# Performance work log

Hardware: AMD Instinct MI355X
Metric: run time of the kernel (lower is better)

## Reference

```python
import jax, jax.numpy as jnp
import numpy as np

N_HEADS, D_MODEL, D_HEAD, N_CTX = 16, 2048, 128, 2048
BATCH, SEQ = 2, 2048
ATTN_SCALE = float(np.sqrt(D_HEAD))
IGNORE = -100000.0


def setup_inputs() -> dict:
    key = jax.random.key(0)
    ks = jax.random.split(key, 6)
    init = 0.02
    return {
        "residual": jax.random.normal(ks[0], (BATCH, SEQ, D_MODEL), dtype=jnp.float32),
        "x": jax.random.normal(ks[1], (BATCH, SEQ, D_MODEL), dtype=jnp.float32),
        "W_Q": jax.random.normal(ks[2], (N_HEADS, D_MODEL, D_HEAD), dtype=jnp.float32) * init,
        "W_K": jax.random.normal(ks[3], (N_HEADS, D_MODEL, D_HEAD), dtype=jnp.float32) * init,
        "W_V": jax.random.normal(ks[4], (N_HEADS, D_MODEL, D_HEAD), dtype=jnp.float32) * init,
        "W_O": jax.random.normal(ks[5], (N_HEADS, D_HEAD, D_MODEL), dtype=jnp.float32) * init,
        "b_Q": jnp.zeros((N_HEADS, D_HEAD), dtype=jnp.float32),
        "b_K": jnp.zeros((N_HEADS, D_HEAD), dtype=jnp.float32),
        "b_V": jnp.zeros((N_HEADS, D_HEAD), dtype=jnp.float32),
        "b_O": jnp.zeros((D_MODEL,), dtype=jnp.float32),
    }


def reference(residual, x, W_Q, W_K, W_V, W_O, b_Q, b_K, b_V, b_O):
    # use_split_qkv_input=False: QKV all read from residual
    q = jnp.einsum('bpm,hmd->bphd', residual, W_Q) + b_Q  # [b, pos, h, d_head]
    k = jnp.einsum('bpm,hmd->bphd', residual, W_K) + b_K
    v = jnp.einsum('bpm,hmd->bphd', residual, W_V) + b_V
    attn_scores = jnp.einsum('bqhd,bkhd->bhqk', q, k) / ATTN_SCALE  # [b, h, q, k]
    key_len = attn_scores.shape[-1]
    mask = jnp.tril(jnp.ones((key_len, key_len), dtype=bool))  # causal mask [q, k]
    attn_scores = jnp.where(mask, attn_scores, IGNORE)
    pattern = jax.nn.softmax(attn_scores, axis=-1)
    z = jnp.einsum('bkhd,bhqk->bqhd', v, pattern)
    out = jnp.einsum('bphd,hdm->bpm', z, W_O) + b_O
    return (residual, out)
```

## Files before the change

### kernel.cpp

```cpp
#include <hip/hip_runtime.h>
#include <hip/hip_bf16.h>

typedef __attribute__((ext_vector_type(8))) short bf16x8;
typedef __attribute__((ext_vector_type(4))) float f32x4;

#define N_HEADS 16
#define D_MODEL 2048
#define D_HEAD  128
#define SEQ     2048
#define BATCH   2
#define HD      (N_HEADS * D_HEAD)
#define QSCALE  0.08838834764831845f

__device__ inline __hip_bfloat16 to_bf16(float v) { return __float2bfloat16(v); }
__device__ inline __hip_bfloat16 to_bf16(__hip_bfloat16 v) { return v; }

typedef __attribute__((address_space(3))) unsigned lds_u32_t;
typedef __attribute__((address_space(1))) unsigned glb_u32_t;
__device__ inline void async16(void* l, const void* g) {
    __builtin_amdgcn_global_load_lds((const glb_u32_t*)g, (lds_u32_t*)l, 16, 0, 0);
}

__global__ __launch_bounds__(256) void cvt_dual(
    const float4* __restrict__ in, float4* __restrict__ o32,
    __hip_bfloat16* __restrict__ obf, long n4)
{
    for (long i = (long)blockIdx.x * blockDim.x + threadIdx.x; i < n4;
         i += (long)gridDim.x * blockDim.x) {
        float4 v = in[i];
        o32[i] = v;
        union { __hip_bfloat16 b[4]; uint2 u; } p;
        p.b[0] = __float2bfloat16(v.x);
        p.b[1] = __float2bfloat16(v.y);
        p.b[2] = __float2bfloat16(v.z);
        p.b[3] = __float2bfloat16(v.w);
        *(uint2*)(obf + 4 * i) = p.u;
    }
}

template <typename Tin>
__global__ __launch_bounds__(256) void transpose_to_bf16(
    const Tin* __restrict__ in, __hip_bfloat16* __restrict__ out,
    int R, int C, long in_rs, long in_bs, long out_bs)
{
    __shared__ Tin tile[64][65];
    const Tin* src = in + (long)blockIdx.z * in_bs;
    __hip_bfloat16* dst = out + (long)blockIdx.z * out_bs;
    const int c0 = blockIdx.x * 64, r0 = blockIdx.y * 64;
    const int t = threadIdx.x;
    const int tr = t >> 4;
    const int tc = (t & 15) * 4;
#pragma unroll
    for (int i = 0; i < 4; i++) {
        int r = tr + i * 16;
#pragma unroll
        for (int j = 0; j < 4; j++)
            tile[r][tc + j] = src[(long)(r0 + r) * in_rs + c0 + tc + j];
    }
    __syncthreads();
#pragma unroll
    for (int i = 0; i < 4; i++) {
        int c = tr + i * 16;
#pragma unroll
        for (int j = 0; j < 4; j++)
            dst[(long)(c0 + c) * R + r0 + tc + j] = to_bf16(tile[tc + j][c]);
    }
}

__device__ inline void store_out(__hip_bfloat16* p, float v) { *p = __float2bfloat16(v); }
__device__ inline void store_out(float* p, float v) { *p = v; }

template <typename OutT>
__global__ __launch_bounds__(256) void gemm_qkv(
    const __hip_bfloat16* __restrict__ A,
    const __hip_bfloat16* __restrict__ WTbase,
    const float* __restrict__ bQ, const float* bK, const float* bV,
    OutT* __restrict__ Cbase,
    int M, int N, int K, long wstride, long cstride, float scale0)
{
    __shared__ __align__(16) __hip_bfloat16 As[128 * 32];
    __shared__ __align__(16) __hip_bfloat16 Bs[128 * 32];
    const int z = blockIdx.z;
    const __hip_bfloat16* Bt = WTbase + (long)z * wstride;
    const float* bias = (z == 0) ? bQ : ((z == 1) ? bK : bV);
    OutT* C = Cbase + (long)z * cstride;
    const float outscale = (z == 0) ? scale0 : 1.0f;

    const int tid = threadIdx.x;
    const int lane = tid & 63, wave = tid >> 6;
    const int l15 = lane & 15, quad = lane >> 4;
    const int wr = wave >> 1, wc = wave & 1;
    const int m0 = blockIdx.y * 128, n0 = blockIdx.x * 128;

    const short* Ap = (const short*)A;
    const short* Bp = (const short*)Bt;

    f32x4 acc[4][4] = {};

    for (int k0 = 0; k0 < K; k0 += 32) {
        __syncthreads();
#pragma unroll
        for (int i = 0; i < 2; i++) {
            int e = i * 256 + tid;
            int row = e >> 2, ch = e & 3;
            async16((char*)As + (i * 256 + wave * 64) * 16,
                    Ap + (long)(m0 + row) * K + k0 + ch * 8);
            async16((char*)Bs + (i * 256 + wave * 64) * 16,
                    Bp + (long)(n0 + row) * K + k0 + ch * 8);
        }
        __syncthreads();

        bf16x8 af[4], bfr[4];
#pragma unroll
        for (int t = 0; t < 4; t++) {
            af[t]  = *(const bf16x8*)((const short*)As + (wr * 64 + t * 16 + l15) * 32 + quad * 8);
            bfr[t] = *(const bf16x8*)((const short*)Bs + (wc * 64 + t * 16 + l15) * 32 + quad * 8);
        }
#pragma unroll
        for (int i = 0; i < 4; i++)
#pragma unroll
            for (int j = 0; j < 4; j++)
                acc[i][j] = __builtin_amdgcn_mfma_f32_16x16x32_bf16(af[i], bfr[j], acc[i][j], 0, 0, 0);
    }

    const int mw = m0 + wr * 64, nw = n0 + wc * 64;
#pragma unroll
    for (int i = 0; i < 4; i++) {
#pragma unroll
        for (int j = 0; j < 4; j++) {
            int n = nw + j * 16 + l15;
            float bv = bias[n];
#pragma unroll
            for (int r = 0; r < 4; r++) {
                int m = mw + i * 16 + quad * 4 + r;
                store_out(&C[(long)m * N + n], (acc[i][j][r] + bv) * outscale);
            }
        }
    }
}

template <typename OutT>
__global__ __launch_bounds__(256, 2) void gemm128(
    const __hip_bfloat16* __restrict__ A,
    const __hip_bfloat16* __restrict__ WTbase,
    const float* __restrict__ bQ, const float* bK, const float* bV,
    OutT* __restrict__ Cbase,
    int N, int K, long wstride, long cstride, float scale0,
    int nx, int ny)
{
    __shared__ __align__(16) short lds[2][2][128 * 64];

    const int tid = threadIdx.x;
    const int lane = tid & 63;
    const int wave = tid >> 6;
    const int l15 = lane & 15, quad = lane >> 4, l7 = lane & 7;
    const int wm = wave >> 1, wn = wave & 1;

    const int nwg = gridDim.x;
    const int orig = blockIdx.x;
    const int wg = (orig & 7) * (nwg >> 3) + (orig >> 3);
    const int nxy = nx * ny;
    const int z = wg / nxy;
    const int rem = wg - z * nxy;
    const int by = rem / nx;
    const int bx = rem - by * nx;
    const int m0 = by * 128, n0 = bx * 128;

    const short* Ap = (const short*)A;
    const short* Bp = (const short*)WTbase + (long)z * wstride;

    const int rsub = lane >> 3;
    const int c0 = (lane & 7) ^ rsub;

    auto stage = [&](int bf, int reg, const short* gbase, int kt) {
        char* base = (char*)&lds[bf][reg][0];
        const short* g = gbase + (long)kt * 64;
#pragma unroll
        for (int s = 0; s < 4; s++) {
            int row = (s * 4 + wave) * 8 + rsub;
            async16(base + (s * 4 + wave) * 1024, g + (long)row * K + c0 * 8);
        }
    };

    const short* Agbl = Ap + (long)m0 * K;
    const short* Bgbl = Bp + (long)n0 * K;

    const int NT = K >> 6;

    stage(0, 0, Agbl, 0); stage(0, 1, Bgbl, 0);
    stage(1, 0, Agbl, 1);
    asm volatile("s_waitcnt vmcnt(4)" ::: "memory");
    __builtin_amdgcn_s_barrier();

    f32x4 acc[4][4] = {};
    const int ar0 = wm * 64;
    const int br0 = wn * 64;

#pragma unroll 2
    for (int u = 0; u < NT; ++u) {
        asm volatile("" ::: "memory");
        const int bf = u & 1, bo = bf ^ 1;
        const short* la = &lds[bf][0][0];
        const short* lb = &lds[bf][1][0];

        bf16x8 a[4][2], b0[2][2], b1[2][2];

#pragma unroll
        for (int fm = 0; fm < 4; fm++)
#pragma unroll
            for (int kk = 0; kk < 2; kk++)
                a[fm][kk] = *(const bf16x8*)(la + (ar0 + fm * 16 + l15) * 64
                                             + (((kk * 4 + quad) ^ l7) * 8));
#pragma unroll
        for (int fn = 0; fn < 2; fn++)
#pragma unroll
            for (int kk = 0; kk < 2; kk++)
                b0[fn][kk] = *(const bf16x8*)(lb + (br0 + fn * 16 + l15) * 64
                                              + (((kk * 4 + quad) ^ l7) * 8));
        if (u + 1 < NT) stage(bo, 1, Bgbl, u + 1);
        __builtin_amdgcn_s_barrier();
        asm volatile("s_waitcnt lgkmcnt(0)" ::: "memory");
        __builtin_amdgcn_sched_barrier(0);
        __builtin_amdgcn_s_setprio(1);
#pragma unroll
        for (int fm = 0; fm < 4; fm++)
#pragma unroll
            for (int fn = 0; fn < 2; fn++)
#pragma unroll
                for (int kk = 0; kk < 2; kk++)
                    acc[fm][fn] = __builtin_amdgcn_mfma_f32_16x16x32_bf16(
                        a[fm][kk], b0[fn][kk], acc[fm][fn], 0, 0, 0);
        __builtin_amdgcn_s_setprio(0);
        __builtin_amdgcn_s_barrier();

#pragma unroll
        for (int fn = 0; fn < 2; fn++)
#pragma unroll
            for (int kk = 0; kk < 2; kk++)
                b1[fn][kk] = *(const bf16x8*)(lb + (br0 + 32 + fn * 16 + l15) * 64
                                              + (((kk * 4 + quad) ^ l7) * 8));
        if (u + 2 < NT) stage(bf, 0, Agbl, u + 2);
        __builtin_amdgcn_s_barrier();
        asm volatile("s_waitcnt lgkmcnt(0)" ::: "memory");
        __builtin_amdgcn_sched_barrier(0);
        __builtin_amdgcn_s_setprio(1);
#pragma unroll
        for (int fm = 0; fm < 4; fm++)
#pragma unroll
            for (int fn = 0; fn < 2; fn++)
#pragma unroll
                for (int kk = 0; kk < 2; kk++)
                    acc[fm][2 + fn] = __builtin_amdgcn_mfma_f32_16x16x32_bf16(
                        a[fm][kk], b1[fn][kk], acc[fm][2 + fn], 0, 0, 0);
        __builtin_amdgcn_s_setprio(0);
        if (u + 2 < NT) {
            asm volatile("s_waitcnt vmcnt(4)" ::: "memory");
        } else if (u + 1 < NT) {
            asm volatile("s_waitcnt vmcnt(0)" ::: "memory");
        }
        __builtin_amdgcn_s_barrier();
    }

    const float* bias = (z == 0) ? bQ : ((z == 1) ? bK : bV);
    OutT* C = Cbase + (long)z * cstride;
    const float outscale = (z == 0) ? scale0 : 1.0f;
#pragma unroll
    for (int mi = 0; mi < 4; mi++) {
#pragma unroll
        for (int nj = 0; nj < 4; nj++) {
            const int n = n0 + wn * 64 + nj * 16 + l15;
            const float bv = bias[n];
#pragma unroll
            for (int r = 0; r < 4; r++) {
                const int m = m0 + wm * 64 + mi * 16 + quad * 4 + r;
                store_out(&C[(long)m * N + n], (acc[mi][nj][r] + bv) * outscale);
            }
        }
    }
}

__global__ __launch_bounds__(512, 4) void attn_fused(
    const __hip_bfloat16* Q,
    const __hip_bfloat16* __restrict__ Kin,
    const __hip_bfloat16* __restrict__ Vt,
    __hip_bfloat16* Z)
{
    __shared__ __align__(16) __hip_bfloat16 Ks[64 * 128];
    __shared__ __align__(16) __hip_bfloat16 Vs[128 * 64];
    __shared__ __align__(16) __hip_bfloat16 pbuf[8][16 * 80];

    const int tid = threadIdx.x;
    const int lane = tid & 63, wave = tid >> 6;
    const int l15 = lane & 15, quad = lane >> 4;
    const int wh = wave >> 2;
    const int rr4 = (wave & 3) * 16 + quad * 4;

    const int g0id = blockIdx.x;
    const int qt = (g0id < 256) ? (15 - (g0id & 15)) : (g0id & 15);
    const int hb = ((g0id >> 4) & 15) + ((g0id >> 8) << 4);
    const int b = hb >> 4, h = hb & 15;

    const short* Qp = (const short*)Q;
    const short* Kp = (const short*)Kin;
    const short* Vp = (const short*)Vt;

    bf16x8 aq[4];
#pragma unroll
    for (int ks = 0; ks < 4; ks++)
        aq[ks] = *(const bf16x8*)(Qp + (long)(b * SEQ + qt * 128 + wave * 16 + l15) * HD
                                  + h * D_HEAD + ks * 32 + quad * 8);

    f32x4 o[8] = {};
    float lsum[4] = {};

    const short* pw = (const short*)pbuf[wave];

    const int ktiles = 2 * qt + 2;
    for (int kt = 0; kt < ktiles; kt++) {
        const int kb = kt * 64;
        __syncthreads();
#pragma unroll
        for (int i = 0; i < 2; i++) {
            int e = i * 512 + tid;
            int row = e >> 4, cc = (e & 15) ^ (row & 7);
            async16((char*)Ks + (size_t)e * 16,
                    Kp + (long)(b * SEQ + kb + row) * HD + h * D_HEAD + cc * 8);
        }
#pragma unroll
        for (int i = 0; i < 2; i++) {
            int e = i * 512 + tid;
            int row = e >> 3, cc = (e & 7) ^ (row & 7);
            async16((char*)Vs + (size_t)e * 16,
                    Vp + ((long)(b * N_HEADS + h) * D_HEAD + row) * SEQ + kb + cc * 8);
        }
        __syncthreads();

        if (kt <= 2 * qt + wh) {
            f32x4 s[4] = {};
#pragma unroll
            for (int nt = 0; nt < 4; nt++)
#pragma unroll
                for (int ks = 0; ks < 4; ks++) {
                    bf16x8 bk = *(const bf16x8*)((const short*)Ks + (nt * 16 + l15) * 128
                                                 + (((ks * 4 + quad) ^ (l15 & 7)) * 8));
                    s[nt] = __builtin_amdgcn_mfma_f32_16x16x32_bf16(aq[ks], bk, s[nt], 0, 0, 0);
                }

            if (kt == 2 * qt + wh) {
#pragma unroll
                for (int nt = 0; nt < 4; nt++)
#pragma unroll
                    for (int r = 0; r < 4; r++) {
                        int kk = nt * 16 + l15;
                        if (kk > rr4 + r) s[nt][r] = -100000.0f;
                    }
            }

#pragma unroll
            for (int nt = 0; nt < 4; nt++)
#pragma unroll
                for (int r = 0; r < 4; r++) {
                    float p = __expf(s[nt][r]);
                    lsum[r] += p;
                    pbuf[wave][(quad * 4 + r) * 80 + nt * 16 + l15] = __float2bfloat16(p);
                }

#pragma unroll
            for (int ks2 = 0; ks2 < 2; ks2++) {
                bf16x8 ap = *(const bf16x8*)(pw + l15 * 80 + ks2 * 32 + quad * 8);
#pragma unroll
                for (int tj = 0; tj < 8; tj++) {
                    bf16x8 bv = *(const bf16x8*)((const short*)Vs + (tj * 16 + l15) * 64
                                                 + (((ks2 * 4 + quad) ^ (l15 & 7)) * 8));
                    o[tj] = __builtin_amdgcn_mfma_f32_16x16x32_bf16(ap, bv, o[tj], 0, 0, 0);
                }
            }
        }
    }

    float inv[4];
#pragma unroll
    for (int r = 0; r < 4; r++) {
        float v = lsum[r];
#pragma unroll
        for (int ofs = 1; ofs < 16; ofs <<= 1)
            v += __shfl_xor(v, ofs, 64);
        inv[r] = 1.0f / v;
    }
#pragma unroll
    for (int tj = 0; tj < 8; tj++)
#pragma unroll
        for (int r = 0; r < 4; r++) {
            long q = b * SEQ + qt * 128 + wave * 16 + quad * 4 + r;
            Z[q * HD + h * D_HEAD + tj * 16 + l15] = __float2bfloat16(o[tj][r] * inv[r]);
        }
}

extern "C" void kernel_launch(void* const* d_in, const int* in_sizes, int n_in,
                              void* d_out, int out_size, void* d_ws, size_t ws_size,
                              hipStream_t stream)
{
    const float* residual = (const float*)d_in[0];
    const float* W_Q = (const float*)d_in[2];
    const float* W_K = (const float*)d_in[3];
    const float* W_V = (const float*)d_in[4];
    const float* W_O = (const float*)d_in[5];
    const float* b_Q = (const float*)d_in[6];
    const float* b_K = (const float*)d_in[7];
    const float* b_V = (const float*)d_in[8];
    const float* b_O = (const float*)d_in[9];
    float* out = (float*)d_out;

    const long TOK = (long)BATCH * SEQ;
    const long TD = TOK * D_MODEL;
    const long WSZ = (long)D_MODEL * D_MODEL;
    char* ws = (char*)d_ws;
    __hip_bfloat16* Qb = (__hip_bfloat16*)(ws);
    __hip_bfloat16* Kb = (__hip_bfloat16*)(ws + TD * 2);
    __hip_bfloat16* Vb = (__hip_bfloat16*)(ws + TD * 4);
    __hip_bfloat16* Rb = (__hip_bfloat16*)(ws + TD * 6);
    __hip_bfloat16* Vt = Rb;
    __hip_bfloat16* WT = (__hip_bfloat16*)(ws + TD * 8);
    __hip_bfloat16* Zb = Qb;

    const size_t NEED_BIG = (size_t)TD * 8 + (size_t)WSZ * 2 * 3;
    const bool big = ws_size >= NEED_BIG;

    dim3 tB(256);

    cvt_dual<<<2048, tB, 0, stream>>>((const float4*)residual, (float4*)out, Rb, TD / 4);

    dim3 gridWqkv(D_HEAD / 64, D_MODEL / 64, N_HEADS);
    const float* Wqkv[3] = {W_Q, W_K, W_V};
    const float* bqkv[3] = {b_Q, b_K, b_V};

    if (big) {
        for (int z = 0; z < 3; z++)
            transpose_to_bf16<float><<<gridWqkv, tB, 0, stream>>>(
                Wqkv[z], WT + (long)z * WSZ, D_MODEL, D_HEAD,
                D_HEAD, (long)D_MODEL * D_HEAD, (long)D_HEAD * D_MODEL);
        gemm128<__hip_bfloat16><<<dim3(1536), dim3(256), 0, stream>>>(
            Rb, WT, b_Q, b_K, b_V, Qb, D_MODEL, D_MODEL,
            WSZ, TD, QSCALE, D_MODEL / 128, (int)(TOK / 128));
    } else {
        dim3 gridG(D_MODEL / 128, (int)(TOK / 128), 1);
        for (int z = 0; z < 3; z++) {
            transpose_to_bf16<float><<<gridWqkv, tB, 0, stream>>>(
                Wqkv[z], WT, D_MODEL, D_HEAD,
                D_HEAD, (long)D_MODEL * D_HEAD, (long)D_HEAD * D_MODEL);
            gemm_qkv<__hip_bfloat16><<<gridG, tB, 0, stream>>>(
                Rb, WT, bqkv[z], bqkv[z], bqkv[z], Qb + (long)z * TD,
                (int)TOK, D_MODEL, D_MODEL, 0, 0, z == 0 ? QSCALE : 1.0f);
        }
    }

    dim3 gridVt(D_HEAD / 64, SEQ / 64, N_HEADS);
    for (int b = 0; b < BATCH; b++) {
        transpose_to_bf16<__hip_bfloat16><<<gridVt, tB, 0, stream>>>(
            Vb + (long)b * SEQ * D_MODEL, Vt + (long)b * N_HEADS * D_HEAD * SEQ,
            SEQ, D_HEAD, (long)D_MODEL, (long)D_HEAD, (long)D_HEAD * SEQ);
    }

    attn_fused<<<dim3(512), dim3(512), 0, stream>>>(Qb, Kb, Vt, Zb);

    dim3 gridWo(D_MODEL / 64, D_MODEL / 64, 1);
    transpose_to_bf16<float><<<gridWo, tB, 0, stream>>>(
        W_O, WT, D_MODEL, D_MODEL, (long)D_MODEL, 0, 0);
    if (big) {
        gemm128<float><<<dim3(512), dim3(256), 0, stream>>>(
            Zb, WT, b_O, b_O, b_O, out + TD, D_MODEL, D_MODEL,
            0, 0, 1.0f, D_MODEL / 128, (int)(TOK / 128));
    } else {
        dim3 gridO(D_MODEL / 128, (int)(TOK / 128), 1);
        gemm_qkv<float><<<gridO, tB, 0, stream>>>(
            Zb, WT, b_O, b_O, b_O, out + TD, (int)TOK, D_MODEL, D_MODEL, 0, 0, 1.0f);
    }
}
```

Measured before the change: 398.2 us.

## Double-buffer K tiles in attention and merge transpose launches

The attention kernel now double-buffers K in shared memory. It prefetches the next K tile and the current V tile asynchronously while QK^T and softmax run, using explicit vmcnt waits and raw barriers in place of two full syncthreads per tile. Separately, the three W_QKV transposes and the per-batch V transposes are each merged into a single launch to cut launch overhead. The pipeline adds 16KB of LDS, which may lower occupancy under the 512x4 launch bounds, and it relies on hand-counted vmcnt values being correct.

```diff
diff --git a/kernel.cpp b/kernel.cpp
--- a/kernel.cpp
+++ b/kernel.cpp
@@ -67,6 +67,67 @@
     }
 }
 
+__global__ __launch_bounds__(256) void transpose_w3(
+    const float* __restrict__ Wq, const float* __restrict__ Wk,
+    const float* __restrict__ Wv, __hip_bfloat16* __restrict__ out)
+{
+    __shared__ float tile[64][65];
+    const int z = blockIdx.z;
+    const int w = z >> 4, hh = z & 15;
+    const float* src = (w == 0 ? Wq : (w == 1 ? Wk : Wv))
+                       + (long)hh * D_MODEL * D_HEAD;
+    __hip_bfloat16* dst = out + (long)w * D_MODEL * D_MODEL
+                          + (long)hh * D_HEAD * D_MODEL;
+    const int c0 = blockIdx.x * 64, r0 = blockIdx.y * 64;
+    const int t = threadIdx.x;
+    const int tr = t >> 4;
+    const int tc = (t & 15) * 4;
+#pragma unroll
+    for (int i = 0; i < 4; i++) {
+        int r = tr + i * 16;
+#pragma unroll
+        for (int j = 0; j < 4; j++)
+            tile[r][tc + j] = src[(long)(r0 + r) * D_HEAD + c0 + tc + j];
+    }
+    __syncthreads();
+#pragma unroll
+    for (int i = 0; i < 4; i++) {
+        int c = tr + i * 16;
+#pragma unroll
+        for (int j = 0; j < 4; j++)
+            dst[(long)(c0 + c) * D_MODEL + r0 + tc + j] = __float2bfloat16(tile[tc + j][c]);
+    }
+}
+
+__global__ __launch_bounds__(256) void transpose_v(
+    const __hip_bfloat16* __restrict__ Vb, __hip_bfloat16* __restrict__ Vt)
+{
+    __shared__ __hip_bfloat16 tile[64][65];
+    const int z = blockIdx.z;
+    const int bb = z >> 4, hh = z & 15;
+    const __hip_bfloat16* src = Vb + (long)bb * SEQ * D_MODEL + hh * D_HEAD;
+    __hip_bfloat16* dst = Vt + ((long)bb * N_HEADS + hh) * (long)D_HEAD * SEQ;
+    const int c0 = blockIdx.x * 64, r0 = blockIdx.y * 64;
+    const int t = threadIdx.x;
+    const int tr = t >> 4;
+    const int tc = (t & 15) * 4;
+#pragma unroll
+    for (int i = 0; i < 4; i++) {
+        int r = tr + i * 16;
+#pragma unroll
+        for (int j = 0; j < 4; j++)
+            tile[r][tc + j] = src[(long)(r0 + r) * D_MODEL + c0 + tc + j];
+    }
+    __syncthreads();
+#pragma unroll
+    for (int i = 0; i < 4; i++) {
+        int c = tr + i * 16;
+#pragma unroll
+        for (int j = 0; j < 4; j++)
+            dst[(long)(c0 + c) * SEQ + r0 + tc + j] = tile[tc + j][c];
+    }
+}
+
 __device__ inline void store_out(__hip_bfloat16* p, float v) { *p = __float2bfloat16(v); }
 __device__ inline void store_out(float* p, float v) { *p = v; }
 
@@ -285,7 +346,7 @@
     const __hip_bfloat16* __restrict__ Vt,
     __hip_bfloat16* Z)
 {
-    __shared__ __align__(16) __hip_bfloat16 Ks[64 * 128];
+    __shared__ __align__(16) __hip_bfloat16 Ks[2][64 * 128];
     __shared__ __align__(16) __hip_bfloat16 Vs[128 * 64];
     __shared__ __align__(16) __hip_bfloat16 pbuf[8][16 * 80];
 
@@ -315,33 +376,48 @@
 
     const short* pw = (const short*)pbuf[wave];
 
-    const int ktiles = 2 * qt + 2;
-    for (int kt = 0; kt < ktiles; kt++) {
-        const int kb = kt * 64;
-        __syncthreads();
+    auto stageK = [&](int buf, int kt) {
 #pragma unroll
         for (int i = 0; i < 2; i++) {
             int e = i * 512 + tid;
             int row = e >> 4, cc = (e & 15) ^ (row & 7);
-            async16((char*)Ks + (size_t)e * 16,
-                    Kp + (long)(b * SEQ + kb + row) * HD + h * D_HEAD + cc * 8);
-        }
+            async16((char*)&Ks[buf][0] + (size_t)e * 16,
+                    Kp + (long)(b * SEQ + kt * 64 + row) * HD + h * D_HEAD + cc * 8);
+        }
+    };
+    auto stageV = [&](int kt) {
 #pragma unroll
         for (int i = 0; i < 2; i++) {
             int e = i * 512 + tid;
             int row = e >> 3, cc = (e & 7) ^ (row & 7);
             async16((char*)Vs + (size_t)e * 16,
-                    Vp + ((long)(b * N_HEADS + h) * D_HEAD + row) * SEQ + kb + cc * 8);
-        }
-        __syncthreads();
-
-        if (kt <= 2 * qt + wh) {
-            f32x4 s[4] = {};
+                    Vp + ((long)(b * N_HEADS + h) * D_HEAD + row) * SEQ + kt * 64 + cc * 8);
+        }
+    };
+
+    const int ktiles = 2 * qt + 2;
+    stageK(0, 0);
+
+    for (int kt = 0; kt < ktiles; kt++) {
+        const int buf = kt & 1;
+        const bool more = (kt + 1 < ktiles);
+
+        stageV(kt);
+        if (more) stageK(buf ^ 1, kt + 1);
+
+        if (more) asm volatile("s_waitcnt vmcnt(4)" ::: "memory");
+        else      asm volatile("s_waitcnt vmcnt(2)" ::: "memory");
+        __builtin_amdgcn_s_barrier();
+        asm volatile("" ::: "memory");
+
+        const bool active = (kt <= 2 * qt + wh);
+        f32x4 s[4] = {};
+        if (active) {
 #pragma unroll
             for (int nt = 0; nt < 4; nt++)
 #pragma unroll
                 for (int ks = 0; ks < 4; ks++) {
-                    bf16x8 bk = *(const bf16x8*)((const short*)Ks + (nt * 16 + l15) * 128
+                    bf16x8 bk = *(const bf16x8*)((const short*)&Ks[buf][0] + (nt * 16 + l15) * 128
                                                  + (((ks * 4 + quad) ^ (l15 & 7)) * 8));
                     s[nt] = __builtin_amdgcn_mfma_f32_16x16x32_bf16(aq[ks], bk, s[nt], 0, 0, 0);
                 }
@@ -364,7 +440,14 @@
                     lsum[r] += p;
                     pbuf[wave][(quad * 4 + r) * 80 + nt * 16 + l15] = __float2bfloat16(p);
                 }
-
+        }
+
+        if (more) asm volatile("s_waitcnt vmcnt(2)" ::: "memory");
+        else      asm volatile("s_waitcnt vmcnt(0)" ::: "memory");
+        __builtin_amdgcn_s_barrier();
+        asm volatile("" ::: "memory");
+
+        if (active) {
 #pragma unroll
             for (int ks2 = 0; ks2 < 2; ks2++) {
                 bf16x8 ap = *(const bf16x8*)(pw + l15 * 80 + ks2 * 32 + quad * 8);
@@ -376,6 +459,9 @@
                 }
             }
         }
+
+        __builtin_amdgcn_s_barrier();
+        asm volatile("" ::: "memory");
     }
 
     float inv[4];
@@ -430,19 +516,15 @@
 
     cvt_dual<<<2048, tB, 0, stream>>>((const float4*)residual, (float4*)out, Rb, TD / 4);
 
-    dim3 gridWqkv(D_HEAD / 64, D_MODEL / 64, N_HEADS);
-    const float* Wqkv[3] = {W_Q, W_K, W_V};
-    const float* bqkv[3] = {b_Q, b_K, b_V};
-
     if (big) {
-        for (int z = 0; z < 3; z++)
-            transpose_to_bf16<float><<<gridWqkv, tB, 0, stream>>>(
-                Wqkv[z], WT + (long)z * WSZ, D_MODEL, D_HEAD,
-                D_HEAD, (long)D_MODEL * D_HEAD, (long)D_HEAD * D_MODEL);
-        gemm128<__hip_bfloat16><<<dim3(1536), dim3(256), 0, stream>>>(
+        transpose_w3<<<dim3(2, 32, 48), tB, 0, stream>>>(W_Q, W_K, W_V, WT);
+        gemm128<__hip_bfloat16><<<dim3(1536), tB, 0, stream>>>(
             Rb, WT, b_Q, b_K, b_V, Qb, D_MODEL, D_MODEL,
             WSZ, TD, QSCALE, D_MODEL / 128, (int)(TOK / 128));
     } else {
+        dim3 gridWqkv(D_HEAD / 64, D_MODEL / 64, N_HEADS);
+        const float* Wqkv[3] = {W_Q, W_K, W_V};
+        const float* bqkv[3] = {b_Q, b_K, b_V};
         dim3 gridG(D_MODEL / 128, (int)(TOK / 128), 1);
         for (int z = 0; z < 3; z++) {
             transpose_to_bf16<float><<<gridWqkv, tB, 0, stream>>>(
@@ -454,12 +536,7 @@
         }
     }
 
-    dim3 gridVt(D_HEAD / 64, SEQ / 64, N_HEADS);
-    for (int b = 0; b < BATCH; b++) {
-        transpose_to_bf16<__hip_bfloat16><<<gridVt, tB, 0, stream>>>(
-            Vb + (long)b * SEQ * D_MODEL, Vt + (long)b * N_HEADS * D_HEAD * SEQ,
-            SEQ, D_HEAD, (long)D_MODEL, (long)D_HEAD, (long)D_HEAD * SEQ);
-    }
+    transpose_v<<<dim3(2, 32, 32), tB, 0, stream>>>(Vb, Vt);
 
     attn_fused<<<dim3(512), dim3(512), 0, stream>>>(Qb, Kb, Vt, Zb);
 
@@ -467,7 +544,7 @@
     transpose_to_bf16<float><<<gridWo, tB, 0, stream>>>(
         W_O, WT, D_MODEL, D_MODEL, (long)D_MODEL, 0, 0);
     if (big) {
-        gemm128<float><<<dim3(512), dim3(256), 0, stream>>>(
+        gemm128<float><<<dim3(512), tB, 0, stream>>>(
             Zb, WT, b_O, b_O, b_O, out + TD, D_MODEL, D_MODEL,
             0, 0, 1.0f, D_MODEL / 128, (int)(TOK / 128));
     } else {
```

Result: faster. 384.6 us (-3.4%).
